# Kernel tuning notes

Hardware: AMD Instinct MI355X
Metric: run time of the kernel (lower is better)

## Reference

```python
import jax, jax.numpy as jnp
import numpy as np

EPS = 1e-6

B, R, S, CSEM = 4, 16384, 48, 4


def setup_inputs() -> dict:
    key = jax.random.key(0)
    k1, k2, k3, k4, k5 = jax.random.split(key, 5)
    colors = jax.random.uniform(k1, (B, R, S, 3), dtype=jnp.float32)
    densities = jax.random.normal(k2, (B, R, S, 1), dtype=jnp.float32)
    # depths must be monotonically increasing along the sample axis
    depths = jnp.sort(jax.random.uniform(k3, (B, R, S, 1), dtype=jnp.float32) * 5.0 + 0.5, axis=2)
    # semantics: per-sample class probabilities in [0,1]
    semantics = jax.nn.softmax(jax.random.normal(k4, (B, R, S, CSEM), dtype=jnp.float32), axis=-1)
    levels = jax.random.randint(k5, (B,), 0, 3, dtype=jnp.int32)
    return {"colors": colors, "densities": densities, "depths": depths,
            "semantics": semantics, "levels": levels}


def reference(colors, densities, depths, semantics, levels):
    dtype = colors.dtype
    # midpoints along the sample axis (dim 2)
    deltas = depths[:, :, 1:] - depths[:, :, :-1]            # [B,R,S-1,1]
    colors_mid = (colors[:, :, :-1] + colors[:, :, 1:]) * 0.5
    densities_mid = (densities[:, :, :-1] + densities[:, :, 1:]) * 0.5
    depths_mid = (depths[:, :, :-1] + depths[:, :, 1:]) * 0.5
    sem_mid = (semantics[:, :, :-1] + semantics[:, :, 1:]) * 0.5

    densities_mid = jax.nn.softplus(densities_mid).astype(dtype)  # activation_factory
    alpha = 1.0 - jnp.exp(-densities_mid * deltas)                # [B,R,S-1,1]

    # per-batch level masking (vectorized version of the python loop)
    lv = levels[:, None, None, None]                              # [B,1,1,1]
    sem0 = sem_mid[..., 0:1]
    sem3 = sem_mid[..., 3:4]
    factor = jnp.where(lv == 1, 1.0 - sem0,
             jnp.where(lv == 2, 1.0 - sem0 - sem3, 1.0))
    alpha = alpha * factor

    # level 1: zero ch0, renormalize ch1..3
    tail = sem_mid[..., 1:]
    sem_l1 = jnp.concatenate(
        [jnp.zeros_like(sem0), (tail + EPS) / (tail.sum(-1, keepdims=True) + EPS)], -1)
    # level 2: zero ch0 and ch3, renormalize ch1..2
    mid2 = sem_mid[..., 1:3]
    sem_l2 = jnp.concatenate(
        [jnp.zeros_like(sem0), (mid2 + EPS) / (mid2.sum(-1, keepdims=True) + EPS),
         jnp.zeros_like(sem3)], -1)
    sem_mid = jnp.where(lv == 1, sem_l1, jnp.where(lv == 2, sem_l2, sem_mid))

    # transmittance via exclusive cumprod along sample axis
    alpha_shifted = jnp.concatenate(
        [jnp.ones_like(alpha[:, :, :1]), 1.0 - alpha + 1e-10], axis=-2)
    weights = (alpha * jnp.cumprod(alpha_shifted, axis=-2)[:, :, :-1]).astype(dtype)

    composite_rgb = jnp.sum(weights * colors_mid, axis=-2)       # [B,R,3]
    composite_depth = jnp.sum(weights * depths_mid, axis=-2)     # [B,R,1]
    composite_semantics = jnp.sum(weights * sem_mid, axis=-2)    # [B,R,CSEM]

    composite_depth = jnp.where(jnp.isnan(composite_depth), jnp.inf, composite_depth).astype(dtype)
    composite_depth = jnp.clip(composite_depth, depths.min(), depths.max())
    return composite_rgb, composite_depth, composite_semantics, weights
```

## Files before the change

### kernel.cpp

```cpp
#include <hip/hip_runtime.h>
#include <math.h>

#define EPSF 1e-6f
#define NB 4
#define NR 16384
#define NS 48
#define NSEG 47
#define NRAYS (NB * NR)
#define KL 16
#define SPL 3
#define RPT 4
#define TPB 64
#define NBLK (NRAYS / RPT)

#define LC 0
#define LSM 576
#define LD 1360
#define LZ 1552
#define LTOT 1760
#define LW LC
#define LP LSM

typedef const __attribute__((address_space(1))) void as1_cvoid;
typedef __attribute__((address_space(3))) void as3_void;

__device__ __forceinline__ float softplus_f(float x) {
    return fmaxf(x, 0.0f) + __logf(1.0f + __expf(-fabsf(x)));
}

__global__ __launch_bounds__(256) void minmax_ends(const float* __restrict__ z,
                                                   float2* __restrict__ ws2) {
    __shared__ float smn[4], smx[4];
    float mn = INFINITY, mx = -INFINITY;
#pragma unroll
    for (int k = 0; k < 4; ++k) {
        const int ray = blockIdx.x * 1024 + k * 256 + threadIdx.x;
        mn = fminf(mn, z[(size_t)ray * NS]);
        mx = fmaxf(mx, z[(size_t)ray * NS + (NS - 1)]);
    }
#pragma unroll
    for (int off = 32; off > 0; off >>= 1) {
        mn = fminf(mn, __shfl_down(mn, off));
        mx = fmaxf(mx, __shfl_down(mx, off));
    }
    if ((threadIdx.x & 63) == 0) {
        smn[threadIdx.x >> 6] = mn;
        smx[threadIdx.x >> 6] = mx;
    }
    __syncthreads();
    if (threadIdx.x == 0) {
        mn = fminf(fminf(smn[0], smn[1]), fminf(smn[2], smn[3]));
        mx = fmaxf(fmaxf(smx[0], smx[1]), fmaxf(smx[2], smx[3]));
        ws2[blockIdx.x] = make_float2(mn, mx);
    }
}

__global__ __launch_bounds__(TPB, 6) void march_kernel(
    const float* __restrict__ colors, const float* __restrict__ densities,
    const float* __restrict__ depths, const float* __restrict__ semantics,
    const int* __restrict__ levels, float* __restrict__ out) {
    __shared__ float lds[LTOT];
    const int lane = threadIdx.x;
    const int r = lane >> 4;
    const int t = lane & 15;
    const int ray0 = blockIdx.x * RPT;
    const int ray = ray0 + r;
    const int lv = levels[ray >> 14];

    {
        const float* c = colors + (size_t)ray0 * 144;
        __builtin_amdgcn_global_load_lds((as1_cvoid*)(c + lane * 4),
                                         (as3_void*)(lds + LC), 16, 0, 0);
        __builtin_amdgcn_global_load_lds((as1_cvoid*)(c + 256 + lane * 4),
                                         (as3_void*)(lds + LC + 256), 16, 0, 0);
        if (lane < 16)
            __builtin_amdgcn_global_load_lds((as1_cvoid*)(c + 512 + lane * 4),
                                             (as3_void*)(lds + LC + 512), 16, 0,
                                             0);
    }
    if (lane < 48) {
#pragma unroll
        for (int rr = 0; rr < RPT; ++rr)
            __builtin_amdgcn_global_load_lds(
                (as1_cvoid*)(semantics + (size_t)(ray0 + rr) * 192 + lane * 4),
                (as3_void*)(lds + LSM + rr * 196), 16, 0, 0);
        __builtin_amdgcn_global_load_lds(
            (as1_cvoid*)(densities + (size_t)ray0 * 48 + lane * 4),
            (as3_void*)(lds + LD), 16, 0, 0);
        __builtin_amdgcn_global_load_lds(
            (as1_cvoid*)(depths + (size_t)ray0 * 48 + lane * 4),
            (as3_void*)(lds + LZ), 16, 0, 0);
    }

    asm volatile("s_waitcnt vmcnt(0)" ::: "memory");

    const int cb = LC + r * 144 + 9 * t;
    const float4* sp = (const float4*)(lds + LSM + r * 196);
    const int db = LD + r * 48 + 3 * t;
    const int zb = LZ + r * 48 + 3 * t;

    float pc0 = lds[cb + 0], pc1 = lds[cb + 1], pc2 = lds[cb + 2];
    float4 psm = sp[3 * t];
    float pdn = lds[db], pz = lds[zb];

    float T = 1.0f;
    float wl[SPL];
    float acc_r = 0.f, acc_g = 0.f, acc_b = 0.f, acc_d = 0.f;
    float acc_s0 = 0.f, acc_s1 = 0.f, acc_s2 = 0.f, acc_s3 = 0.f;

#pragma unroll
    for (int j = 0; j < SPL; ++j) {
        float c0 = lds[cb + 3 * (j + 1)];
        float c1 = lds[cb + 3 * (j + 1) + 1];
        float c2 = lds[cb + 3 * (j + 1) + 2];
        float4 sm4 = sp[3 * t + j + 1];
        float dn = lds[db + j + 1];
        float z = lds[zb + j + 1];

        wl[j] = 0.0f;
        if (j < 2 || t < 15) {
            float delta = z - pz;
            float cm0 = (pc0 + c0) * 0.5f;
            float cm1 = (pc1 + c1) * 0.5f;
            float cm2 = (pc2 + c2) * 0.5f;
            float dnm = (pdn + dn) * 0.5f;
            float zm = (pz + z) * 0.5f;
            float sm0 = (psm.x + sm4.x) * 0.5f;
            float sm1 = (psm.y + sm4.y) * 0.5f;
            float sm2 = (psm.z + sm4.z) * 0.5f;
            float sm3 = (psm.w + sm4.w) * 0.5f;

            float sp_ = softplus_f(dnm);
            float alpha = 1.0f - __expf(-sp_ * delta);

            float factor, o0, o1, o2, o3;
            if (lv == 1) {
                factor = 1.0f - sm0;
                float inv = 1.0f / (sm1 + sm2 + sm3 + EPSF);
                o0 = 0.0f;
                o1 = (sm1 + EPSF) * inv;
                o2 = (sm2 + EPSF) * inv;
                o3 = (sm3 + EPSF) * inv;
            } else if (lv == 2) {
                factor = 1.0f - sm0 - sm3;
                float inv = 1.0f / (sm1 + sm2 + EPSF);
                o0 = 0.0f;
                o1 = (sm1 + EPSF) * inv;
                o2 = (sm2 + EPSF) * inv;
                o3 = 0.0f;
            } else {
                factor = 1.0f;
                o0 = sm0; o1 = sm1; o2 = sm2; o3 = sm3;
            }

            alpha *= factor;
            float w = alpha * T;
            T *= (1.0f - alpha + 1e-10f);
            wl[j] = w;

            acc_r += w * cm0;
            acc_g += w * cm1;
            acc_b += w * cm2;
            acc_d += w * zm;
            acc_s0 += w * o0;
            acc_s1 += w * o1;
            acc_s2 += w * o2;
            acc_s3 += w * o3;
        }
        pc0 = c0; pc1 = c1; pc2 = c2;
        psm = sm4; pdn = dn; pz = z;
    }

    float p = T;
#pragma unroll
    for (int off = 1; off < KL; off <<= 1) {
        float u = __shfl_up(p, off, KL);
        if (t >= off) p *= u;
    }
    float Tstart = __shfl_up(p, 1, KL);
    if (t == 0) Tstart = 1.0f;

    acc_r *= Tstart; acc_g *= Tstart; acc_b *= Tstart; acc_d *= Tstart;
    acc_s0 *= Tstart; acc_s1 *= Tstart; acc_s2 *= Tstart; acc_s3 *= Tstart;

#pragma unroll
    for (int j = 0; j < SPL; ++j) {
        if (j < 2 || t < 15)
            lds[LW + r * NSEG + 3 * t + j] = wl[j] * Tstart;
    }

    {
        const int pb = LP + r * 144 + t * 9;
        lds[pb + 0] = acc_r;  lds[pb + 1] = acc_g;
        lds[pb + 2] = acc_b;  lds[pb + 3] = acc_d;
        lds[pb + 4] = acc_s0; lds[pb + 5] = acc_s1;
        lds[pb + 6] = acc_s2; lds[pb + 7] = acc_s3;
    }

    if (lane < 47) {
        const float4* src = (const float4*)(lds + LW);
        float4* dst = (float4*)(out + (size_t)NRAYS * 8 + (size_t)ray0 * NSEG);
        dst[lane] = src[lane];
    }

    if (lane < 32) {
        const int rr = lane >> 3, qq = lane & 7;
        const int qb = LP + rr * 144 + qq;
        float v = 0.0f;
#pragma unroll
        for (int k = 0; k < KL; ++k) v += lds[qb + 9 * k];

        const int oray = ray0 + rr;
        size_t oidx;
        if (qq < 3) {
            oidx = (size_t)oray * 3 + qq;
        } else if (qq == 3) {
            if (isnan(v)) v = INFINITY;
            oidx = (size_t)NRAYS * 3 + oray;
        } else {
            oidx = (size_t)NRAYS * 4 + (size_t)oray * 4 + (qq - 4);
        }
        out[oidx] = v;
    }
}

__global__ __launch_bounds__(256) void clip_depth(const float2* __restrict__ ws2,
                                                  float* __restrict__ dout) {
    __shared__ float smn[4], smx[4];
    float mn = INFINITY, mx = -INFINITY;
    if (threadIdx.x < 64) {
        float2 v = ws2[threadIdx.x];
        mn = v.x;
        mx = v.y;
    }
#pragma unroll
    for (int off = 32; off > 0; off >>= 1) {
        mn = fminf(mn, __shfl_down(mn, off));
        mx = fmaxf(mx, __shfl_down(mx, off));
    }
    if ((threadIdx.x & 63) == 0) {
        smn[threadIdx.x >> 6] = mn;
        smx[threadIdx.x >> 6] = mx;
    }
    __syncthreads();
    mn = fminf(fminf(smn[0], smn[1]), fminf(smn[2], smn[3]));
    mx = fmaxf(fmaxf(smx[0], smx[1]), fmaxf(smx[2], smx[3]));

    float4* d4 = (float4*)dout;
    const int i = blockIdx.x * 256 + threadIdx.x;
    float4 v = d4[i];
    v.x = fminf(fmaxf(v.x, mn), mx);
    v.y = fminf(fmaxf(v.y, mn), mx);
    v.z = fminf(fmaxf(v.z, mn), mx);
    v.w = fminf(fmaxf(v.w, mn), mx);
    d4[i] = v;
}

extern "C" void kernel_launch(void* const* d_in, const int* in_sizes, int n_in,
                              void* d_out, int out_size, void* d_ws, size_t ws_size,
                              hipStream_t stream) {
    const float* colors = (const float*)d_in[0];
    const float* densities = (const float*)d_in[1];
    const float* depths = (const float*)d_in[2];
    const float* semantics = (const float*)d_in[3];
    const int* levels = (const int*)d_in[4];
    float* out = (float*)d_out;
    float2* ws2 = (float2*)d_ws;

    minmax_ends<<<64, 256, 0, stream>>>(depths, ws2);
    march_kernel<<<NBLK, TPB, 0, stream>>>(colors, densities, depths, semantics,
                                           levels, out);
    clip_depth<<<64, 256, 0, stream>>>(ws2, out + (size_t)NRAYS * 3);
}
```

Baseline: 32.80 us.

## Double-buffer LDS tiles across persistent blocks and fuse depth min/max into march

Each block now processes 8 four-ray tiles in sequence instead of one. While the current tile is computed, global_load_lds prefetches the next tile into a second LDS buffer, and partial s_waitcnt counts keep that load in flight. The separate minmax_ends kernel is removed: per-block depth min/max is computed from LDS and written to workspace, and clip_depth reduces more entries. This cuts one launch and hides load latency, but there are 8x fewer blocks, occupancy is lower because of doubled LDS and dropped launch bounds, and correctness depends on hand-tuned vmcnt values.

```diff
diff --git a/kernel.cpp b/kernel.cpp
--- a/kernel.cpp
+++ b/kernel.cpp
@@ -11,13 +11,14 @@
 #define SPL 3
 #define RPT 4
 #define TPB 64
-#define NBLK (NRAYS / RPT)
+#define TPBLK 8
+#define NBLK (NRAYS / (RPT * TPBLK))
 
 #define LC 0
 #define LSM 576
-#define LD 1360
-#define LZ 1552
-#define LTOT 1760
+#define LD 1344
+#define LZ 1536
+#define BUFSZ 1744
 #define LW LC
 #define LP LSM
 
@@ -28,74 +29,49 @@
     return fmaxf(x, 0.0f) + __logf(1.0f + __expf(-fabsf(x)));
 }
 
-__global__ __launch_bounds__(256) void minmax_ends(const float* __restrict__ z,
-                                                   float2* __restrict__ ws2) {
-    __shared__ float smn[4], smx[4];
-    float mn = INFINITY, mx = -INFINITY;
-#pragma unroll
-    for (int k = 0; k < 4; ++k) {
-        const int ray = blockIdx.x * 1024 + k * 256 + threadIdx.x;
-        mn = fminf(mn, z[(size_t)ray * NS]);
-        mx = fmaxf(mx, z[(size_t)ray * NS + (NS - 1)]);
-    }
-#pragma unroll
-    for (int off = 32; off > 0; off >>= 1) {
-        mn = fminf(mn, __shfl_down(mn, off));
-        mx = fmaxf(mx, __shfl_down(mx, off));
-    }
-    if ((threadIdx.x & 63) == 0) {
-        smn[threadIdx.x >> 6] = mn;
-        smx[threadIdx.x >> 6] = mx;
-    }
-    __syncthreads();
-    if (threadIdx.x == 0) {
-        mn = fminf(fminf(smn[0], smn[1]), fminf(smn[2], smn[3]));
-        mx = fmaxf(fmaxf(smx[0], smx[1]), fmaxf(smx[2], smx[3]));
-        ws2[blockIdx.x] = make_float2(mn, mx);
-    }
-}
-
-__global__ __launch_bounds__(TPB, 6) void march_kernel(
-    const float* __restrict__ colors, const float* __restrict__ densities,
-    const float* __restrict__ depths, const float* __restrict__ semantics,
-    const int* __restrict__ levels, float* __restrict__ out) {
-    __shared__ float lds[LTOT];
-    const int lane = threadIdx.x;
-    const int r = lane >> 4;
-    const int t = lane & 15;
-    const int ray0 = blockIdx.x * RPT;
-    const int ray = ray0 + r;
-    const int lv = levels[ray >> 14];
-
-    {
-        const float* c = colors + (size_t)ray0 * 144;
-        __builtin_amdgcn_global_load_lds((as1_cvoid*)(c + lane * 4),
-                                         (as3_void*)(lds + LC), 16, 0, 0);
-        __builtin_amdgcn_global_load_lds((as1_cvoid*)(c + 256 + lane * 4),
-                                         (as3_void*)(lds + LC + 256), 16, 0, 0);
-        if (lane < 16)
-            __builtin_amdgcn_global_load_lds((as1_cvoid*)(c + 512 + lane * 4),
-                                             (as3_void*)(lds + LC + 512), 16, 0,
-                                             0);
-    }
+__device__ __forceinline__ void stage(const float* __restrict__ colors,
+                                      const float* __restrict__ semantics,
+                                      const float* __restrict__ densities,
+                                      const float* __restrict__ depths,
+                                      int tile, float* buf, int lane) {
+    const int ray0 = tile * RPT;
+    const float* c = colors + (size_t)ray0 * 144;
+    __builtin_amdgcn_global_load_lds((as1_cvoid*)(c + lane * 4),
+                                     (as3_void*)(buf + LC), 16, 0, 0);
+    __builtin_amdgcn_global_load_lds((as1_cvoid*)(c + 256 + lane * 4),
+                                     (as3_void*)(buf + LC + 256), 16, 0, 0);
+    if (lane < 16)
+        __builtin_amdgcn_global_load_lds((as1_cvoid*)(c + 512 + lane * 4),
+                                         (as3_void*)(buf + LC + 512), 16, 0, 0);
+    const float* s = semantics + (size_t)ray0 * 192;
+#pragma unroll
+    for (int i = 0; i < 3; ++i)
+        __builtin_amdgcn_global_load_lds((as1_cvoid*)(s + i * 256 + lane * 4),
+                                         (as3_void*)(buf + LSM + i * 256), 16, 0,
+                                         0);
     if (lane < 48) {
-#pragma unroll
-        for (int rr = 0; rr < RPT; ++rr)
-            __builtin_amdgcn_global_load_lds(
-                (as1_cvoid*)(semantics + (size_t)(ray0 + rr) * 192 + lane * 4),
-                (as3_void*)(lds + LSM + rr * 196), 16, 0, 0);
         __builtin_amdgcn_global_load_lds(
             (as1_cvoid*)(densities + (size_t)ray0 * 48 + lane * 4),
-            (as3_void*)(lds + LD), 16, 0, 0);
+            (as3_void*)(buf + LD), 16, 0, 0);
         __builtin_amdgcn_global_load_lds(
             (as1_cvoid*)(depths + (size_t)ray0 * 48 + lane * 4),
-            (as3_void*)(lds + LZ), 16, 0, 0);
-    }
-
-    asm volatile("s_waitcnt vmcnt(0)" ::: "memory");
+            (as3_void*)(buf + LZ), 16, 0, 0);
+    }
+}
+
+__device__ __forceinline__ void do_tile(const float* lds, int tile, int lv,
+                                        float* __restrict__ out, float& gmn,
+                                        float& gmx, int lane, int r, int t,
+                                        float* ldsw) {
+    const int ray0 = tile * RPT;
+
+    if (lane < 4) {
+        gmn = fminf(gmn, lds[LZ + lane * 48]);
+        gmx = fmaxf(gmx, lds[LZ + lane * 48 + 47]);
+    }
 
     const int cb = LC + r * 144 + 9 * t;
-    const float4* sp = (const float4*)(lds + LSM + r * 196);
+    const float4* sp = (const float4*)(lds + LSM + r * 192);
     const int db = LD + r * 48 + 3 * t;
     const int zb = LZ + r * 48 + 3 * t;
 
@@ -186,15 +162,15 @@
 #pragma unroll
     for (int j = 0; j < SPL; ++j) {
         if (j < 2 || t < 15)
-            lds[LW + r * NSEG + 3 * t + j] = wl[j] * Tstart;
+            ldsw[LW + r * NSEG + 3 * t + j] = wl[j] * Tstart;
     }
 
     {
         const int pb = LP + r * 144 + t * 9;
-        lds[pb + 0] = acc_r;  lds[pb + 1] = acc_g;
-        lds[pb + 2] = acc_b;  lds[pb + 3] = acc_d;
-        lds[pb + 4] = acc_s0; lds[pb + 5] = acc_s1;
-        lds[pb + 6] = acc_s2; lds[pb + 7] = acc_s3;
+        ldsw[pb + 0] = acc_r;  ldsw[pb + 1] = acc_g;
+        ldsw[pb + 2] = acc_b;  ldsw[pb + 3] = acc_d;
+        ldsw[pb + 4] = acc_s0; ldsw[pb + 5] = acc_s1;
+        ldsw[pb + 6] = acc_s2; ldsw[pb + 7] = acc_s3;
     }
 
     if (lane < 47) {
@@ -224,14 +200,56 @@
     }
 }
 
+__global__ __launch_bounds__(TPB) void march_kernel(
+    const float* __restrict__ colors, const float* __restrict__ densities,
+    const float* __restrict__ depths, const float* __restrict__ semantics,
+    const int* __restrict__ levels, float2* __restrict__ ws2,
+    float* __restrict__ out) {
+    __shared__ float lds[2 * BUFSZ];
+    const int lane = threadIdx.x;
+    const int r = lane >> 4;
+    const int t = lane & 15;
+    const int tile0 = blockIdx.x * TPBLK;
+    const int lv = levels[(tile0 * RPT) >> 14];
+    float gmn = INFINITY, gmx = -INFINITY;
+
+    stage(colors, semantics, densities, depths, tile0, lds, lane);
+
+    stage(colors, semantics, densities, depths, tile0 + 1, lds + BUFSZ, lane);
+    asm volatile("" ::: "memory");
+    asm volatile("s_waitcnt vmcnt(8)" ::: "memory");
+    do_tile(lds, tile0, lv, out, gmn, gmx, lane, r, t, lds);
+
+#pragma unroll 2
+    for (int k = 1; k < TPBLK - 1; ++k) {
+        float* nbuf = lds + (((k + 1) & 1) ? BUFSZ : 0);
+        float* cbuf = lds + ((k & 1) ? BUFSZ : 0);
+        stage(colors, semantics, densities, depths, tile0 + k + 1, nbuf, lane);
+        asm volatile("" ::: "memory");
+        asm volatile("s_waitcnt vmcnt(10)" ::: "memory");
+        do_tile(cbuf, tile0 + k, lv, out, gmn, gmx, lane, r, t, cbuf);
+    }
+
+    asm volatile("s_waitcnt vmcnt(2)" ::: "memory");
+    do_tile(lds + BUFSZ, tile0 + TPBLK - 1, lv, out, gmn, gmx, lane, r, t,
+            lds + BUFSZ);
+
+    gmn = fminf(gmn, __shfl_xor(gmn, 1, 4));
+    gmn = fminf(gmn, __shfl_xor(gmn, 2, 4));
+    gmx = fmaxf(gmx, __shfl_xor(gmx, 1, 4));
+    gmx = fmaxf(gmx, __shfl_xor(gmx, 2, 4));
+    if (lane == 0) ws2[blockIdx.x] = make_float2(gmn, gmx);
+}
+
 __global__ __launch_bounds__(256) void clip_depth(const float2* __restrict__ ws2,
                                                   float* __restrict__ dout) {
     __shared__ float smn[4], smx[4];
     float mn = INFINITY, mx = -INFINITY;
-    if (threadIdx.x < 64) {
-        float2 v = ws2[threadIdx.x];
-        mn = v.x;
-        mx = v.y;
+#pragma unroll
+    for (int k = 0; k < NBLK / 256; ++k) {
+        float2 v = ws2[threadIdx.x + (k << 8)];
+        mn = fminf(mn, v.x);
+        mx = fmaxf(mx, v.y);
     }
 #pragma unroll
     for (int off = 32; off > 0; off >>= 1) {
@@ -267,8 +285,7 @@
     float* out = (float*)d_out;
     float2* ws2 = (float2*)d_ws;
 
-    minmax_ends<<<64, 256, 0, stream>>>(depths, ws2);
     march_kernel<<<NBLK, TPB, 0, stream>>>(colors, densities, depths, semantics,
-                                           levels, out);
+                                           levels, ws2, out);
     clip_depth<<<64, 256, 0, stream>>>(ws2, out + (size_t)NRAYS * 3);
 }
```

New measurement: 28.88 us. -12.0%, faster.
